# Performance work log

Measured on AMD Instinct MI355X. Metric: run time of the kernel, lower is better.

## Reference

```python
import jax, jax.numpy as jnp
import numpy as np

EMB = 1024
HEADS = 16
HEAD_DIM = EMB // HEADS
FF = 4 * EMB
EPS = 1e-5


def setup_inputs() -> dict:
    key = jax.random.key(0)
    ks = jax.random.split(key, 16)
    s = 0.02
    return {
        "x": jax.random.normal(ks[0], (2, 2048, EMB), dtype=jnp.float32),
        "ln1_g": jnp.ones((EMB,), jnp.float32),
        "ln1_b": jnp.zeros((EMB,), jnp.float32),
        "Wq": jax.random.normal(ks[1], (EMB, EMB), jnp.float32) * s,
        "bq": jnp.zeros((EMB,), jnp.float32),
        "Wk": jax.random.normal(ks[2], (EMB, EMB), jnp.float32) * s,
        "bk": jnp.zeros((EMB,), jnp.float32),
        "Wv": jax.random.normal(ks[3], (EMB, EMB), jnp.float32) * s,
        "bv": jnp.zeros((EMB,), jnp.float32),
        "Wo": jax.random.normal(ks[4], (EMB, EMB), jnp.float32) * s,
        "bo": jnp.zeros((EMB,), jnp.float32),
        "ln2_g": jnp.ones((EMB,), jnp.float32),
        "ln2_b": jnp.zeros((EMB,), jnp.float32),
        "W1": jax.random.normal(ks[5], (EMB, FF), jnp.float32) * s,
        "b1": jnp.zeros((FF,), jnp.float32),
        "W2": jax.random.normal(ks[6], (FF, EMB), jnp.float32) * s,
        "b2": jnp.zeros((EMB,), jnp.float32),
    }


def _layernorm(x, g, b):
    mu = jnp.mean(x, axis=-1, keepdims=True)
    var = jnp.var(x, axis=-1, keepdims=True)
    return (x - mu) * jax.lax.rsqrt(var + EPS) * g + b


def _attention(x, Wq, bq, Wk, bk, Wv, bv, Wo, bo):
    B, T, C = x.shape
    # [B,T,C] -> [B,H,T,Dh]
    def split(y):
        return y.reshape(B, T, HEADS, HEAD_DIM).transpose(0, 2, 1, 3)
    Q = split(x @ Wq + bq)
    K = split(x @ Wk + bk)
    V = split(x @ Wv + bv)
    att = jnp.einsum("bhqd,bhkd->bhqk", Q, K) / np.sqrt(HEAD_DIM).astype(np.float32)
    causal = jnp.tril(jnp.ones((T, T), bool))
    att = jnp.where(causal, att, -jnp.inf)
    att = jax.nn.softmax(att, axis=-1)
    out = jnp.einsum("bhqk,bhkd->bhqd", att, V)
    out = out.transpose(0, 2, 1, 3).reshape(B, T, C)
    return out @ Wo + bo


def reference(x, ln1_g, ln1_b, Wq, bq, Wk, bk, Wv, bv, Wo, bo,
              ln2_g, ln2_b, W1, b1, W2, b2):
    # dropout is identity in eval mode
    x = x + _attention(_layernorm(x, ln1_g, ln1_b), Wq, bq, Wk, bk, Wv, bv, Wo, bo)
    h = _layernorm(x, ln2_g, ln2_b)
    h = jax.nn.gelu(h @ W1 + b1, approximate=False) @ W2 + b2
    return x + h
```

## Files before the change

kernel.cpp:

```cpp
#include <hip/hip_runtime.h>
#include <hip/hip_bf16.h>

typedef __attribute__((ext_vector_type(4))) float f32x4;
typedef __attribute__((ext_vector_type(8))) short bf16x8;
typedef unsigned int u32;
typedef unsigned short u16;

#define GASP __attribute__((address_space(1)))
#define LASP __attribute__((address_space(3)))

__device__ __forceinline__ u16 f2bf(float f) {
  u32 u = __float_as_uint(f);
  return (u16)((u + 0x7fffu + ((u >> 16) & 1u)) >> 16);
}

__device__ __forceinline__ void gl_lds16(const void* g, void* l) {
  __builtin_amdgcn_global_load_lds((const GASP u32*)g, (LASP u32*)l, 16, 0, 0);
}

struct CastArgs {
  const float* s[6];
  u16* d[6];
};

__global__ __launch_bounds__(256) void cast_w(CastArgs a) {
  int bid = blockIdx.x;
  int w, t, K, N, kshift;
  if (bid < 4096)      { w = bid >> 10; t = bid & 1023; K = 1024; N = 1024; kshift = 5; }
  else if (bid < 8192) { w = 4; t = bid - 4096; K = 1024; N = 4096; kshift = 5; }
  else                 { w = 5; t = bid - 8192; K = 4096; N = 1024; kshift = 7; }
  int tk = t & ((1 << kshift) - 1);
  int tn = t >> kshift;
  int k0 = tk << 5, n0 = tn << 5;
  const float* src = a.s[w];
  u16* dst = a.d[w];
  __shared__ u16 tile[32][36];
  int r = threadIdx.x >> 3, c0 = (threadIdx.x & 7) << 2;
  float4 v = *(const float4*)&src[(size_t)(k0 + r) * N + n0 + c0];
  tile[c0 + 0][r] = f2bf(v.x);
  tile[c0 + 1][r] = f2bf(v.y);
  tile[c0 + 2][r] = f2bf(v.z);
  tile[c0 + 3][r] = f2bf(v.w);
  __syncthreads();
  ushort4 o;
  o.x = tile[r][c0 + 0];
  o.y = tile[r][c0 + 1];
  o.z = tile[r][c0 + 2];
  o.w = tile[r][c0 + 3];
  *(ushort4*)&dst[(size_t)(n0 + r) * K + k0 + c0] = o;
}

__global__ __launch_bounds__(256) void ln_k(const float* __restrict__ x, const float* __restrict__ g,
                                            const float* __restrict__ b, u16* __restrict__ out) {
  int row = blockIdx.x;
  int tid = threadIdx.x;
  float4 v = *(const float4*)&x[(size_t)row * 1024 + tid * 4];
  float s = v.x + v.y + v.z + v.w;
  float ss = v.x * v.x + v.y * v.y + v.z * v.z + v.w * v.w;
#pragma unroll
  for (int o = 32; o >= 1; o >>= 1) {
    s += __shfl_xor(s, o, 64);
    ss += __shfl_xor(ss, o, 64);
  }
  __shared__ float red[8];
  int wv = tid >> 6;
  if ((tid & 63) == 0) { red[wv] = s; red[wv + 4] = ss; }
  __syncthreads();
  s = red[0] + red[1] + red[2] + red[3];
  ss = red[4] + red[5] + red[6] + red[7];
  float mu = s * (1.0f / 1024.0f);
  float var = ss * (1.0f / 1024.0f) - mu * mu;
  float rstd = rsqrtf(var + 1e-5f);
  float4 gv = *(const float4*)&g[tid * 4];
  float4 bv = *(const float4*)&b[tid * 4];
  ushort4 o4;
  o4.x = f2bf((v.x - mu) * rstd * gv.x + bv.x);
  o4.y = f2bf((v.y - mu) * rstd * gv.y + bv.y);
  o4.z = f2bf((v.z - mu) * rstd * gv.z + bv.z);
  o4.w = f2bf((v.w - mu) * rstd * gv.w + bv.w);
  *(ushort4*)&out[(size_t)row * 1024 + tid * 4] = o4;
}

template <int MODE>
__global__ __launch_bounds__(256) void gemm_bt(
    const u16* __restrict__ A, const u16* __restrict__ Bt,
    const float* __restrict__ bias0, const float* __restrict__ bias1, const float* __restrict__ bias2,
    void* outp, const float* res, int M, int N, int K) {
  __shared__ __align__(16) u16 As[2][128 * 32];
  __shared__ __align__(16) u16 Bs[2][128 * 32];
  const int tid = threadIdx.x;
  const int w = tid >> 6, lane = tid & 63;
  const int m0 = blockIdx.y << 7, n0 = blockIdx.x << 7;

  const u16* aS[2];
  const u16* bS[2];
  char* asB = (char*)As;
  char* bsB = (char*)Bs;
#pragma unroll
  for (int i = 0; i < 2; ++i) {
    int p = w * 2048 + i * 1024 + lane * 16;
    int r = p >> 6;
    int cl = ((p >> 4) & 3) ^ ((r >> 1) & 3);
    aS[i] = A + (size_t)(m0 + r) * K + cl * 8;
    bS[i] = Bt + (size_t)(n0 + r) * K + cl * 8;
  }
  f32x4 acc[4][4];
#pragma unroll
  for (int i = 0; i < 4; ++i)
#pragma unroll
    for (int j = 0; j < 4; ++j) acc[i][j] = f32x4{0.f, 0.f, 0.f, 0.f};

  const int wr = w >> 1, wc = w & 1;
  int aOff[4], bOff[4];
#pragma unroll
  for (int mm = 0; mm < 4; ++mm) {
    int rowa = wr * 64 + mm * 16 + (lane & 15);
    aOff[mm] = rowa * 64 + (((lane >> 4) ^ ((rowa >> 1) & 3)) << 4);
    int rowb = wc * 64 + mm * 16 + (lane & 15);
    bOff[mm] = rowb * 64 + (((lane >> 4) ^ ((rowb >> 1) & 3)) << 4);
  }

  gl_lds16(aS[0], asB + w * 2048);
  gl_lds16(aS[1], asB + w * 2048 + 1024);
  gl_lds16(bS[0], bsB + w * 2048);
  gl_lds16(bS[1], bsB + w * 2048 + 1024);
  int buf = 0;
  for (int ks = 0; ks < K; ks += 32) {
    __syncthreads();
    if (ks + 32 < K) {
      const int nb = (buf ^ 1) * 8192;
      gl_lds16(aS[0] + ks + 32, asB + nb + w * 2048);
      gl_lds16(aS[1] + ks + 32, asB + nb + w * 2048 + 1024);
      gl_lds16(bS[0] + ks + 32, bsB + nb + w * 2048);
      gl_lds16(bS[1] + ks + 32, bsB + nb + w * 2048 + 1024);
    }
    const int tb = buf * 8192;
    bf16x8 av[4], bv[4];
#pragma unroll
    for (int mm = 0; mm < 4; ++mm) av[mm] = *(const bf16x8*)(asB + tb + aOff[mm]);
#pragma unroll
    for (int nn = 0; nn < 4; ++nn) bv[nn] = *(const bf16x8*)(bsB + tb + bOff[nn]);
#pragma unroll
    for (int mm = 0; mm < 4; ++mm)
#pragma unroll
      for (int nn = 0; nn < 4; ++nn)
        acc[mm][nn] = __builtin_amdgcn_mfma_f32_16x16x32_bf16(av[mm], bv[nn], acc[mm][nn], 0, 0, 0);
    buf ^= 1;
  }

  const int g = lane >> 4, ci = lane & 15;
#pragma unroll
  for (int mm = 0; mm < 4; ++mm) {
#pragma unroll
    for (int nn = 0; nn < 4; ++nn) {
      int colb = n0 + wc * 64 + nn * 16 + ci;
      int rowbase = m0 + wr * 64 + mm * 16 + 4 * g;
      f32x4 c = acc[mm][nn];
      if constexpr (MODE == 2) {
        int sel = colb >> 10;
        int cc = colb & 1023;
        const float* bp = sel == 0 ? bias0 : (sel == 1 ? bias1 : bias2);
        float bb = bp[cc];
        int h = cc >> 6, d = cc & 63;
        int b_ = rowbase >> 11, tt = rowbase & 2047;
        if (sel == 2) {
          u16* op = (u16*)outp + 2ull * (4096ull * 1024ull);
          ushort4 o4;
          o4.x = f2bf(c[0] + bb);
          o4.y = f2bf(c[1] + bb);
          o4.z = f2bf(c[2] + bb);
          o4.w = f2bf(c[3] + bb);
          *(ushort4*)&op[((size_t)(b_ * 16 + h) * 64 + d) * 2048 + tt] = o4;
        } else {
          float scale = (sel == 0) ? 0.125f : 1.0f;
          u16* op = (u16*)outp + (size_t)sel * (4096ull * 1024ull);
#pragma unroll
          for (int r = 0; r < 4; ++r)
            op[((size_t)(b_ * 16 + h) * 2048 + tt + r) * 64 + d] = f2bf((c[r] + bb) * scale);
        }
      } else {
        float bb = bias0[colb];
#pragma unroll
        for (int r = 0; r < 4; ++r) {
          float v = c[r] + bb;
          float gl = 0.5f * v * (1.0f + erff(v * 0.70710678118654752f));
          ((u16*)outp)[(size_t)(rowbase + r) * N + colb] = f2bf(gl);
        }
      }
    }
  }
}

__global__ __launch_bounds__(512) void gemm_sk(
    const u16* __restrict__ A, const u16* __restrict__ Bt,
    const float* __restrict__ bias0, float* __restrict__ outp,
    const float* __restrict__ res, int M, int N, int K) {
  __shared__ __align__(16) union SM {
    struct { u16 As[2][2][128 * 32]; u16 Bs[2][2][128 * 32]; } t;
    float red[16][4][4][64];
  } sm;
  const int tid = threadIdx.x;
  const int w8 = tid >> 6, lane = tid & 63;
  const int gg = w8 >> 2, wl = w8 & 3;
  const int m0 = blockIdx.y << 7, n0 = blockIdx.x << 7;

  char* asB = (char*)sm.t.As[gg];
  char* bsB = (char*)sm.t.Bs[gg];
  const u16* aS[2];
  const u16* bS[2];
#pragma unroll
  for (int i = 0; i < 2; ++i) {
    int p = wl * 2048 + i * 1024 + lane * 16;
    int r = p >> 6;
    int cl = ((p >> 4) & 3) ^ ((r >> 1) & 3);
    aS[i] = A + (size_t)(m0 + r) * K + gg * 32 + cl * 8;
    bS[i] = Bt + (size_t)(n0 + r) * K + gg * 32 + cl * 8;
  }
  f32x4 acc[4][4];
#pragma unroll
  for (int i = 0; i < 4; ++i)
#pragma unroll
    for (int j = 0; j < 4; ++j) acc[i][j] = f32x4{0.f, 0.f, 0.f, 0.f};

  const int wr = wl >> 1, wc = wl & 1;
  int aOff[4], bOff[4];
#pragma unroll
  for (int mm = 0; mm < 4; ++mm) {
    int rowa = wr * 64 + mm * 16 + (lane & 15);
    aOff[mm] = rowa * 64 + (((lane >> 4) ^ ((rowa >> 1) & 3)) << 4);
    int rowb = wc * 64 + mm * 16 + (lane & 15);
    bOff[mm] = rowb * 64 + (((lane >> 4) ^ ((rowb >> 1) & 3)) << 4);
  }

  gl_lds16(aS[0], asB + wl * 2048);
  gl_lds16(aS[1], asB + wl * 2048 + 1024);
  gl_lds16(bS[0], bsB + wl * 2048);
  gl_lds16(bS[1], bsB + wl * 2048 + 1024);
  int buf = 0;
  for (int ks = 0; ks < K; ks += 64) {
    __syncthreads();
    if (ks + 64 < K) {
      const int nb = (buf ^ 1) * 8192;
      gl_lds16(aS[0] + ks + 64, asB + nb + wl * 2048);
      gl_lds16(aS[1] + ks + 64, asB + nb + wl * 2048 + 1024);
      gl_lds16(bS[0] + ks + 64, bsB + nb + wl * 2048);
      gl_lds16(bS[1] + ks + 64, bsB + nb + wl * 2048 + 1024);
    }
    const int tb = buf * 8192;
    bf16x8 av[4], bv[4];
#pragma unroll
    for (int mm = 0; mm < 4; ++mm) av[mm] = *(const bf16x8*)(asB + tb + aOff[mm]);
#pragma unroll
    for (int nn = 0; nn < 4; ++nn) bv[nn] = *(const bf16x8*)(bsB + tb + bOff[nn]);
#pragma unroll
    for (int mm = 0; mm < 4; ++mm)
#pragma unroll
      for (int nn = 0; nn < 4; ++nn)
        acc[mm][nn] = __builtin_amdgcn_mfma_f32_16x16x32_bf16(av[mm], bv[nn], acc[mm][nn], 0, 0, 0);
    buf ^= 1;
  }

  __syncthreads();
  if (gg == 1) {
#pragma unroll
    for (int mm = 0; mm < 4; ++mm)
#pragma unroll
      for (int nn = 0; nn < 4; ++nn)
#pragma unroll
        for (int r = 0; r < 4; ++r) sm.red[mm * 4 + nn][r][wl][lane] = acc[mm][nn][r];
  }
  __syncthreads();
  if (gg == 0) {
    const int g = lane >> 4, ci = lane & 15;
#pragma unroll
    for (int mm = 0; mm < 4; ++mm) {
#pragma unroll
      for (int nn = 0; nn < 4; ++nn) {
        int colb = n0 + wc * 64 + nn * 16 + ci;
        int rowbase = m0 + wr * 64 + mm * 16 + 4 * g;
        float bb = bias0[colb];
#pragma unroll
        for (int r = 0; r < 4; ++r) {
          size_t idx = (size_t)(rowbase + r) * N + colb;
          outp[idx] = acc[mm][nn][r] + sm.red[mm * 4 + nn][r][wl][lane] + bb + res[idx];
        }
      }
    }
  }
}

__global__ __launch_bounds__(256) void attn_k(const u16* __restrict__ Q, const u16* __restrict__ Kg,
                                              const u16* __restrict__ Vt, u16* __restrict__ O) {
  __shared__ __align__(16) u16 Ks[2][64 * 64];
  __shared__ __align__(16) u16 Vs[2][64 * 64];
  const int bx = blockIdx.x;
  const int bh = blockIdx.y;
  const int tid = threadIdx.x, w = tid >> 6, lane = tid & 63;
  const int g = lane >> 4, qi = lane & 15;
  const u16* Qb = Q + (size_t)bh * 2048 * 64;
  const u16* Kb = Kg + (size_t)bh * 2048 * 64;
  const u16* Vtb = Vt + (size_t)bh * 64 * 2048;

  const int rl8 = lane >> 3;
  const int cs = ((lane & 7) ^ rl8) * 8;
  const u16* srcK0 = Kb + (size_t)(16 * w + rl8) * 64 + cs;
  const u16* srcK1 = srcK0 + 8 * 64;
  const u16* srcV0 = Vtb + (size_t)(16 * w + rl8) * 2048 + cs;
  const u16* srcV1 = srcV0 + 8 * 2048;
  char* ksB = (char*)Ks;
  char* vsB = (char*)Vs;
  const int dstOff = w * 2048 + lane * 16;

  int koff[4][2], voff[4][2];
#pragma unroll
  for (int t = 0; t < 4; ++t) {
    int row = 16 * t + qi;
#pragma unroll
    for (int h = 0; h < 2; ++h) koff[t][h] = row * 128 + (((4 * h + g) ^ (qi & 7)) << 4);
#pragma unroll
    for (int kt = 0; kt < 2; ++kt) voff[t][kt] = row * 128 + (((4 * kt + g) ^ (qi & 7)) << 4);
  }

  const int b_ = bh >> 4, hh = bh & 15;
  u32* Ou = (u32*)O;

  for (int job = 0; job < 2; ++job) {
    const int qt = job ? bx : 31 - bx;
    const int qrow = qt * 64 + w * 16 + qi;

    bf16x8 qf[2];
#pragma unroll
    for (int h = 0; h < 2; ++h)
      qf[h] = *(const bf16x8*)(Qb + (size_t)qrow * 64 + h * 32 + g * 8);

    f32x4 acc[4];
#pragma unroll
    for (int dt = 0; dt < 4; ++dt) acc[dt] = f32x4{0.f, 0.f, 0.f, 0.f};
    float m = -1e30f, lsum = 0.0f;

    __syncthreads();
    gl_lds16(srcK0, ksB + dstOff);
    gl_lds16(srcK1, ksB + dstOff + 1024);
    gl_lds16(srcV0, vsB + dstOff);
    gl_lds16(srcV1, vsB + dstOff + 1024);

    int buf = 0;
    for (int s = 0; s <= qt; ++s) {
      __syncthreads();
      if (s < qt) {
        int nb = buf ^ 1;
        gl_lds16(srcK0 + (size_t)(s + 1) * 4096, ksB + nb * 8192 + dstOff);
        gl_lds16(srcK1 + (size_t)(s + 1) * 4096, ksB + nb * 8192 + dstOff + 1024);
        gl_lds16(srcV0 + (size_t)(s + 1) * 64, vsB + nb * 8192 + dstOff);
        gl_lds16(srcV1 + (size_t)(s + 1) * 64, vsB + nb * 8192 + dstOff + 1024);
      }
      const int tb = buf * 8192;
      f32x4 st[4];
      __builtin_amdgcn_s_setprio(1);
#pragma unroll
      for (int t = 0; t < 4; ++t) {
        st[t] = f32x4{0.f, 0.f, 0.f, 0.f};
#pragma unroll
        for (int h = 0; h < 2; ++h) {
          bf16x8 kf = *(const bf16x8*)(ksB + tb + koff[t][h]);
          st[t] = __builtin_amdgcn_mfma_f32_16x16x32_bf16(kf, qf[h], st[t], 0, 0, 0);
        }
      }
      __builtin_amdgcn_s_setprio(0);
      float pvv[4][4];
      float tmax = -1e30f;
      if (s == qt) {
#pragma unroll
        for (int t = 0; t < 4; ++t)
#pragma unroll
          for (int r = 0; r < 4; ++r) {
            int key = 64 * s + 16 * t + 4 * g + r;
            float sv = st[t][r];
            sv = (key <= qrow) ? sv : -1e30f;
            pvv[t][r] = sv;
            tmax = fmaxf(tmax, sv);
          }
      } else {
#pragma unroll
        for (int t = 0; t < 4; ++t)
#pragma unroll
          for (int r = 0; r < 4; ++r) {
            float sv = st[t][r];
            pvv[t][r] = sv;
            tmax = fmaxf(tmax, sv);
          }
      }
      tmax = fmaxf(tmax, __shfl_xor(tmax, 16, 64));
      tmax = fmaxf(tmax, __shfl_xor(tmax, 32, 64));
      float mn = fmaxf(m, tmax);
      float corr = __expf(m - mn);
      float tsum = 0.f;
#pragma unroll
      for (int t = 0; t < 4; ++t)
#pragma unroll
        for (int r = 0; r < 4; ++r) {
          float e = __expf(pvv[t][r] - mn);
          pvv[t][r] = e;
          tsum += e;
        }
      tsum += __shfl_xor(tsum, 16, 64);
      tsum += __shfl_xor(tsum, 32, 64);
      lsum = lsum * corr + tsum;
      m = mn;
#pragma unroll
      for (int dt = 0; dt < 4; ++dt)
#pragma unroll
        for (int r = 0; r < 4; ++r) acc[dt][r] *= corr;
      u32 pk[4][2], ex[4][2];
#pragma unroll
      for (int t = 0; t < 4; ++t)
#pragma unroll
        for (int p = 0; p < 2; ++p) {
          u32 v = (u32)f2bf(pvv[t][2 * p]) | ((u32)f2bf(pvv[t][2 * p + 1]) << 16);
          pk[t][p] = v;
          ex[t][p] = (u32)__shfl_xor((int)v, 16, 64);
        }
      const bool ge = (g & 1) == 0;
      const bool G0 = (g >> 1) == 0;
      const bool innr = (g == 0) || (g == 3);
      u32 mm_[4][4];
#pragma unroll
      for (int t = 0; t < 4; ++t) {
        mm_[t][0] = ge ? pk[t][0] : ex[t][0];
        mm_[t][1] = ge ? pk[t][1] : ex[t][1];
        mm_[t][2] = ge ? ex[t][0] : pk[t][0];
        mm_[t][3] = ge ? ex[t][1] : pk[t][1];
      }
      union Frag { u32 u[4]; bf16x8 v; } f0, f1;
#pragma unroll
      for (int i = 0; i < 4; ++i) {
        u32 sel0 = G0 ? mm_[1][i] : mm_[0][i];
        u32 sel1 = G0 ? mm_[3][i] : mm_[2][i];
        u32 sw0 = (u32)__shfl_xor((int)sel0, 32, 64);
        u32 sw1 = (u32)__shfl_xor((int)sel1, 32, 64);
        u32 own0 = G0 ? mm_[0][i] : mm_[1][i];
        u32 own1 = G0 ? mm_[2][i] : mm_[3][i];
        f0.u[i] = innr ? own0 : sw0;
        f1.u[i] = innr ? own1 : sw1;
      }
      __builtin_amdgcn_s_setprio(1);
#pragma unroll
      for (int dt = 0; dt < 4; ++dt) {
        bf16x8 vfa = *(const bf16x8*)(vsB + tb + voff[dt][0]);
        acc[dt] = __builtin_amdgcn_mfma_f32_16x16x32_bf16(vfa, f0.v, acc[dt], 0, 0, 0);
        bf16x8 vfb = *(const bf16x8*)(vsB + tb + voff[dt][1]);
        acc[dt] = __builtin_amdgcn_mfma_f32_16x16x32_bf16(vfb, f1.v, acc[dt], 0, 0, 0);
      }
      __builtin_amdgcn_s_setprio(0);
      buf ^= 1;
    }

    float rl = 1.0f / lsum;
    size_t rowq = (size_t)(b_ * 2048 + qrow);
#pragma unroll
    for (int dt = 0; dt < 4; ++dt) {
#pragma unroll
      for (int rp = 0; rp < 2; ++rp) {
        u16 lo = f2bf(acc[dt][rp * 2] * rl);
        u16 hi = f2bf(acc[dt][rp * 2 + 1] * rl);
        u32 pkd = (u32)lo | ((u32)hi << 16);
        size_t off = rowq * 1024 + hh * 64 + dt * 16 + 4 * g + rp * 2;
        Ou[off >> 1] = pkd;
      }
    }
  }
}

extern "C" void kernel_launch(void* const* d_in, const int* in_sizes, int n_in,
                              void* d_out, int out_size, void* d_ws, size_t ws_size,
                              hipStream_t stream) {
  const float* x    = (const float*)d_in[0];
  const float* ln1g = (const float*)d_in[1];
  const float* ln1b = (const float*)d_in[2];
  const float* Wq   = (const float*)d_in[3];
  const float* bq   = (const float*)d_in[4];
  const float* Wk   = (const float*)d_in[5];
  const float* bk   = (const float*)d_in[6];
  const float* Wv   = (const float*)d_in[7];
  const float* bv   = (const float*)d_in[8];
  const float* Wo   = (const float*)d_in[9];
  const float* bo   = (const float*)d_in[10];
  const float* ln2g = (const float*)d_in[11];
  const float* ln2b = (const float*)d_in[12];
  const float* W1   = (const float*)d_in[13];
  const float* b1   = (const float*)d_in[14];
  const float* W2   = (const float*)d_in[15];
  const float* b2   = (const float*)d_in[16];

  char* ws = (char*)d_ws;
  const size_t MB = 1ull << 20;
  u16* WqT = (u16*)(ws + 0 * MB);
  u16* WkT = (u16*)(ws + 2 * MB);
  u16* WvT = (u16*)(ws + 4 * MB);
  u16* WoT = (u16*)(ws + 6 * MB);
  u16* W1T = (u16*)(ws + 8 * MB);
  u16* W2T = (u16*)(ws + 16 * MB);
  u16* XN  = (u16*)(ws + 24 * MB);
  u16* Qb  = (u16*)(ws + 32 * MB);
  u16* Kb  = (u16*)(ws + 40 * MB);
  u16* Vtb = (u16*)(ws + 48 * MB);
  u16* Ob  = (u16*)(ws + 56 * MB);
  u16* Gb  = (u16*)(ws + 32 * MB);

  CastArgs ca;
  ca.s[0] = Wq; ca.s[1] = Wk; ca.s[2] = Wv; ca.s[3] = Wo; ca.s[4] = W1; ca.s[5] = W2;
  ca.d[0] = WqT; ca.d[1] = WkT; ca.d[2] = WvT; ca.d[3] = WoT; ca.d[4] = W1T; ca.d[5] = W2T;
  cast_w<<<12288, 256, 0, stream>>>(ca);

  ln_k<<<4096, 256, 0, stream>>>(x, ln1g, ln1b, XN);

  gemm_bt<2><<<dim3(24, 32), 256, 0, stream>>>(XN, WqT, bq, bk, bv, Qb, nullptr, 4096, 3072, 1024);

  attn_k<<<dim3(16, 32), 256, 0, stream>>>(Qb, Kb, Vtb, Ob);

  gemm_sk<<<dim3(8, 32), 512, 0, stream>>>(Ob, WoT, bo, (float*)d_out, x, 4096, 1024, 1024);

  ln_k<<<4096, 256, 0, stream>>>((const float*)d_out, ln2g, ln2b, XN);

  gemm_bt<3><<<dim3(32, 32), 256, 0, stream>>>(XN, W1T, b1, nullptr, nullptr, Gb, nullptr, 4096, 4096, 1024);

  gemm_sk<<<dim3(8, 32), 512, 0, stream>>>(Gb, W2T, b2, (float*)d_out, (const float*)d_out, 4096, 1024, 4096);
}
```

Measured before the change: 269.4 us.

## Triple-buffer GEMM LDS tiles with explicit vmcnt waits and barriers

```diff
diff --git a/kernel.cpp b/kernel.cpp
--- a/kernel.cpp
+++ b/kernel.cpp
@@ -86,8 +86,8 @@
     const u16* __restrict__ A, const u16* __restrict__ Bt,
     const float* __restrict__ bias0, const float* __restrict__ bias1, const float* __restrict__ bias2,
     void* outp, const float* res, int M, int N, int K) {
-  __shared__ __align__(16) u16 As[2][128 * 32];
-  __shared__ __align__(16) u16 Bs[2][128 * 32];
+  __shared__ __align__(16) u16 As[3][128 * 32];
+  __shared__ __align__(16) u16 Bs[3][128 * 32];
   const int tid = threadIdx.x;
   const int w = tid >> 6, lane = tid & 63;
   const int m0 = blockIdx.y << 7, n0 = blockIdx.x << 7;
@@ -124,15 +124,24 @@
   gl_lds16(aS[1], asB + w * 2048 + 1024);
   gl_lds16(bS[0], bsB + w * 2048);
   gl_lds16(bS[1], bsB + w * 2048 + 1024);
+  if (K > 32) {
+    gl_lds16(aS[0] + 32, asB + 8192 + w * 2048);
+    gl_lds16(aS[1] + 32, asB + 8192 + w * 2048 + 1024);
+    gl_lds16(bS[0] + 32, bsB + 8192 + w * 2048);
+    gl_lds16(bS[1] + 32, bsB + 8192 + w * 2048 + 1024);
+  }
   int buf = 0;
   for (int ks = 0; ks < K; ks += 32) {
-    __syncthreads();
-    if (ks + 32 < K) {
-      const int nb = (buf ^ 1) * 8192;
-      gl_lds16(aS[0] + ks + 32, asB + nb + w * 2048);
-      gl_lds16(aS[1] + ks + 32, asB + nb + w * 2048 + 1024);
-      gl_lds16(bS[0] + ks + 32, bsB + nb + w * 2048);
-      gl_lds16(bS[1] + ks + 32, bsB + nb + w * 2048 + 1024);
+    if (ks + 32 >= K) { asm volatile("s_waitcnt vmcnt(0)" ::: "memory"); }
+    else              { asm volatile("s_waitcnt vmcnt(4)" ::: "memory"); }
+    __builtin_amdgcn_s_barrier();
+    asm volatile("" ::: "memory");
+    if (ks + 64 < K) {
+      const int nb = ((buf + 2) % 3) * 8192;
+      gl_lds16(aS[0] + ks + 64, asB + nb + w * 2048);
+      gl_lds16(aS[1] + ks + 64, asB + nb + w * 2048 + 1024);
+      gl_lds16(bS[0] + ks + 64, bsB + nb + w * 2048);
+      gl_lds16(bS[1] + ks + 64, bsB + nb + w * 2048 + 1024);
     }
     const int tb = buf * 8192;
     bf16x8 av[4], bv[4];
@@ -145,7 +154,8 @@
 #pragma unroll
       for (int nn = 0; nn < 4; ++nn)
         acc[mm][nn] = __builtin_amdgcn_mfma_f32_16x16x32_bf16(av[mm], bv[nn], acc[mm][nn], 0, 0, 0);
-    buf ^= 1;
+    buf = buf + 1;
+    if (buf == 3) buf = 0;
   }
 
   const int g = lane >> 4, ci = lane & 15;
@@ -196,7 +206,7 @@
     const float* __restrict__ bias0, float* __restrict__ outp,
     const float* __restrict__ res, int M, int N, int K) {
   __shared__ __align__(16) union SM {
-    struct { u16 As[2][2][128 * 32]; u16 Bs[2][2][128 * 32]; } t;
+    struct { u16 As[2][3][128 * 32]; u16 Bs[2][3][128 * 32]; } t;
     float red[16][4][4][64];
   } sm;
   const int tid = threadIdx.x;
@@ -236,15 +246,24 @@
   gl_lds16(aS[1], asB + wl * 2048 + 1024);
   gl_lds16(bS[0], bsB + wl * 2048);
   gl_lds16(bS[1], bsB + wl * 2048 + 1024);
+  if (K > 64) {
+    gl_lds16(aS[0] + 64, asB + 8192 + wl * 2048);
+    gl_lds16(aS[1] + 64, asB + 8192 + wl * 2048 + 1024);
+    gl_lds16(bS[0] + 64, bsB + 8192 + wl * 2048);
+    gl_lds16(bS[1] + 64, bsB + 8192 + wl * 2048 + 1024);
+  }
   int buf = 0;
   for (int ks = 0; ks < K; ks += 64) {
-    __syncthreads();
-    if (ks + 64 < K) {
-      const int nb = (buf ^ 1) * 8192;
-      gl_lds16(aS[0] + ks + 64, asB + nb + wl * 2048);
-      gl_lds16(aS[1] + ks + 64, asB + nb + wl * 2048 + 1024);
-      gl_lds16(bS[0] + ks + 64, bsB + nb + wl * 2048);
-      gl_lds16(bS[1] + ks + 64, bsB + nb + wl * 2048 + 1024);
+    if (ks + 64 >= K) { asm volatile("s_waitcnt vmcnt(0)" ::: "memory"); }
+    else              { asm volatile("s_waitcnt vmcnt(4)" ::: "memory"); }
+    __builtin_amdgcn_s_barrier();
+    asm volatile("" ::: "memory");
+    if (ks + 128 < K) {
+      const int nb = ((buf + 2) % 3) * 8192;
+      gl_lds16(aS[0] + ks + 128, asB + nb + wl * 2048);
+      gl_lds16(aS[1] + ks + 128, asB + nb + wl * 2048 + 1024);
+      gl_lds16(bS[0] + ks + 128, bsB + nb + wl * 2048);
+      gl_lds16(bS[1] + ks + 128, bsB + nb + wl * 2048 + 1024);
     }
     const int tb = buf * 8192;
     bf16x8 av[4], bv[4];
@@ -257,7 +276,8 @@
 #pragma unroll
       for (int nn = 0; nn < 4; ++nn)
         acc[mm][nn] = __builtin_amdgcn_mfma_f32_16x16x32_bf16(av[mm], bv[nn], acc[mm][nn], 0, 0, 0);
-    buf ^= 1;
+    buf = buf + 1;
+    if (buf == 3) buf = 0;
   }
 
   __syncthreads();
```

Measured after the change: 252.5 us. 6.3% less time.
